# Performance work log

Hardware: AMD Instinct MI355X
Metric: run time of the kernel (lower is better)

## Reference

```python
import jax, jax.numpy as jnp
import numpy as np

B, S, D, H = 1, 4096, 1024, 16
HD = D // H

def setup_inputs() -> dict:
    key = jax.random.key(0)
    ks = jax.random.split(key, 6)
    scale = 0.02
    return {
        "x":  jax.random.normal(ks[0], (B, S, D), dtype=jnp.float32),
        "Wq": jax.random.normal(ks[1], (D, D), dtype=jnp.float32) * scale,
        "Wk": jax.random.normal(ks[2], (D, D), dtype=jnp.float32) * scale,
        "Wv": jax.random.normal(ks[3], (D, D), dtype=jnp.float32) * scale,
        "Wo": jax.random.normal(ks[4], (D, D), dtype=jnp.float32) * scale,
        "bo": jnp.zeros((D,), dtype=jnp.float32),
    }

def reference(x, Wq, Wk, Wv, Wo, bo):
    b, s, d = x.shape
    # torch Linear: y = x @ W.T (weights stored [out,in])
    def proj(W):
        return (x @ W.T).reshape(b, s, H, HD).transpose(0, 2, 1, 3)  # [b,h,s,hd]
    q, k, v = proj(Wq), proj(Wk), proj(Wv)
    scores = jnp.einsum('bhqd,bhkd->bhqk', q, k)  # [b,h,s,s]
    causal = jnp.tril(jnp.ones((s, s), dtype=bool))
    scores = jnp.where(causal, scores, -jnp.inf)
    weights = jax.nn.softmax(scores / np.sqrt(HD).astype(np.float32), axis=-1)
    ctx = jnp.einsum('bhqk,bhkd->bhqd', weights, v)
    ctx = ctx.transpose(0, 2, 1, 3).reshape(b, s, d)
    return ctx @ Wo.T + bo
```

## Files before the change

kernel.cpp:

```cpp
#include <hip/hip_runtime.h>
#include <stdint.h>

typedef unsigned short u16;
typedef __attribute__((ext_vector_type(4))) unsigned short u16x4;
typedef __attribute__((ext_vector_type(8))) unsigned short u16x8;
typedef __attribute__((ext_vector_type(8))) __bf16 bf16x8;
typedef __attribute__((ext_vector_type(4))) float f32x4;

#define S_LEN 4096
#define D_DIM 1024
#define NH    16
#define HD    64

__device__ __forceinline__ u16 f2bf(float f) {
  return __builtin_bit_cast(u16, (__bf16)f);
}
__device__ __forceinline__ float bf2f(u16 v) {
  return __builtin_bit_cast(float, (uint32_t)v << 16);
}
__device__ __forceinline__ bf16x8 bc(u16x8 v) { return __builtin_bit_cast(bf16x8, v); }
__device__ __forceinline__ float fexp2(float x) { return __builtin_amdgcn_exp2f(x); }

__device__ __forceinline__ void gload16(const u16* g, u16* l) {
  __builtin_amdgcn_global_load_lds((__attribute__((address_space(1))) void*)g,
                                   (__attribute__((address_space(3))) void*)l, 16, 0, 0);
}

__global__ __launch_bounds__(256) void conv_kernel(const float* __restrict__ src,
                                                   u16* __restrict__ dst, int n4) {
  int i = blockIdx.x * 256 + threadIdx.x;
  if (i >= n4) return;
  f32x4 v = ((const f32x4*)src)[i];
  u16x4 o;
  o[0] = f2bf(v[0]); o[1] = f2bf(v[1]); o[2] = f2bf(v[2]); o[3] = f2bf(v[3]);
  ((u16x4*)dst)[i] = o;
}

__device__ __forceinline__ void gemm_core(const u16* __restrict__ A,
                                          const u16* __restrict__ W,
                                          int m0, int n0, int Kd,
                                          u16* As, u16* Bs, f32x4 acc[4][4]) {
  const int tid  = threadIdx.x;
  const int lane = tid & 63;
  const int wv   = tid >> 6;
  const int wr   = wv >> 1, wc = wv & 1;
  const int b    = lane & 15, quad = lane >> 4;
  const int lrow = lane >> 2, lkc = (lane & 3) * 8;

  const u16* ga0 = A + (size_t)(m0 + wv * 16 + lrow) * Kd + lkc;
  const u16* ga1 = A + (size_t)(m0 + 64 + wv * 16 + lrow) * Kd + lkc;
  const u16* gb0 = W + (size_t)(n0 + wv * 16 + lrow) * Kd + lkc;
  const u16* gb1 = W + (size_t)(n0 + 64 + wv * 16 + lrow) * Kd + lkc;
  u16* la0 = As + wv * 512;
  u16* la1 = As + 2048 + wv * 512;
  u16* lb0 = Bs + wv * 512;
  u16* lb1 = Bs + 2048 + wv * 512;

  for (int k0 = 0; k0 < Kd; k0 += 32) {
    gload16(ga0 + k0, la0);
    gload16(ga1 + k0, la1);
    gload16(gb0 + k0, lb0);
    gload16(gb1 + k0, lb1);
    __syncthreads();

    u16x8 af[4], bw[4];
#pragma unroll
    for (int i = 0; i < 4; ++i) {
      af[i] = *(const u16x8*)(As + (wr * 64 + i * 16 + b) * 32 + quad * 8);
      bw[i] = *(const u16x8*)(Bs + (wc * 64 + i * 16 + b) * 32 + quad * 8);
    }
#pragma unroll
    for (int i = 0; i < 4; ++i)
#pragma unroll
      for (int j = 0; j < 4; ++j)
        acc[i][j] = __builtin_amdgcn_mfma_f32_16x16x32_bf16(bc(af[i]), bc(bw[j]), acc[i][j], 0, 0, 0);
    __syncthreads();
  }
}

__global__ __launch_bounds__(256) void gemm_qkv_kernel(const u16* __restrict__ X,
                                                       const u16* __restrict__ Wq,
                                                       const u16* __restrict__ Wk,
                                                       const u16* __restrict__ Wv,
                                                       u16* __restrict__ Q,
                                                       u16* __restrict__ K,
                                                       u16* __restrict__ Vt) {
  __shared__ __align__(16) u16 As[128 * 32];
  __shared__ __align__(16) u16 Bs[128 * 32];
  const int z = blockIdx.z;
  const u16* W = (z == 0) ? Wq : (z == 1) ? Wk : Wv;
  const int n0 = blockIdx.x * 128, m0 = blockIdx.y * 128;

  const f32x4 zero4 = {0.f, 0.f, 0.f, 0.f};
  f32x4 acc[4][4];
#pragma unroll
  for (int i = 0; i < 4; ++i)
#pragma unroll
    for (int j = 0; j < 4; ++j) acc[i][j] = zero4;

  gemm_core(X, W, m0, n0, D_DIM, As, Bs, acc);

  const int lane = threadIdx.x & 63;
  const int wv = threadIdx.x >> 6, wr = wv >> 1, wc = wv & 1;
  const int b = lane & 15, quad = lane >> 4;

  if (z < 2) {
    u16* out = (z == 0) ? Q : K;
    const float sc = (z == 0) ? 0.18033688011112042f : 1.0f;
#pragma unroll
    for (int i = 0; i < 4; ++i)
#pragma unroll
      for (int j = 0; j < 4; ++j)
#pragma unroll
        for (int r = 0; r < 4; ++r) {
          int row = m0 + wr * 64 + i * 16 + quad * 4 + r;
          int col = n0 + wc * 64 + j * 16 + b;
          out[(size_t)row * D_DIM + col] = f2bf(acc[i][j][r] * sc);
        }
  } else {
#pragma unroll
    for (int i = 0; i < 4; ++i)
#pragma unroll
      for (int j = 0; j < 4; ++j) {
        int col = n0 + wc * 64 + j * 16 + b;
        int row = m0 + wr * 64 + i * 16 + quad * 4;
        u16x4 vv;
#pragma unroll
        for (int r = 0; r < 4; ++r) vv[r] = f2bf(acc[i][j][r]);
        *(u16x4*)(Vt + (size_t)col * S_LEN + row) = vv;
      }
  }
}

__global__ __launch_bounds__(256) void attn_kernel(const u16* __restrict__ Q,
                                                   const u16* __restrict__ K,
                                                   const u16* __restrict__ Vt,
                                                   u16* __restrict__ Opart,
                                                   float* __restrict__ ml) {
  const int u = (int)gridDim.x - 1 - (int)blockIdx.x;
  const int h = u / 160;
  const int uu = u - h * 160;
  int qt, c;
  if (uu < 16)      { qt = uu;                c = 0; }
  else if (uu < 48) { qt = 16 + ((uu - 16) >> 1); c = (uu - 16) & 1; }
  else if (uu < 96) { qt = 32 + (uu - 48) / 3;    c = (uu - 48) % 3; }
  else              { qt = 48 + ((uu - 96) >> 2); c = (uu - 96) & 3; }
  const int t0 = c * 16;
  const int t_end = min(t0 + 16, qt + 1);
  const int q0 = qt * 64;

  const int tid = threadIdx.x, lane = tid & 63, w = tid >> 6;
  const int quad = lane >> 4, b = lane & 15;
  const int lrow = lane >> 2, lkc = (lane & 3) * 8;

  __shared__ __align__(16) u16 Ks[2 * 4096];
  __shared__ __align__(16) u16 Vts[2 * 4096];
  __shared__ __align__(16) u16 Ps[4][16 * 72];

  u16x8 bq[2];
  {
    const size_t qbase = (size_t)(q0 + w * 16 + b) * D_DIM + h * HD + quad * 8;
    bq[0] = *(const u16x8*)(Q + qbase);
    bq[1] = *(const u16x8*)(Q + qbase + 32);
  }

  const f32x4 zero4 = {0.f, 0.f, 0.f, 0.f};
  f32x4 o[4];
#pragma unroll
  for (int jt = 0; jt < 4; ++jt) o[jt] = zero4;
  float m_run = -3.0e38f, l_run = 0.f;

  auto stage = [&](int t, int bsel) {
    const int kv0s = t * 64;
    const u16* kg = K + (size_t)(kv0s + w * 16 + lrow) * D_DIM + h * HD + lkc;
    const u16* vg = Vt + (size_t)(h * HD + w * 16 + lrow) * S_LEN + kv0s + lkc;
    u16* kbase = Ks + bsel * 4096 + w * 512;
    u16* vbase = Vts + bsel * 4096 + w * 512;
    gload16(kg, kbase);
    gload16(kg + 32, kbase + 2048);
    gload16(vg, vbase);
    gload16(vg + 32, vbase + 2048);
  };

  u16* PsW = &Ps[w][0];
  stage(t0, 0);
  int buf = 0;

  for (int t = t0; t < t_end; ++t) {
    __syncthreads();
    if (t + 1 < t_end) stage(t + 1, buf ^ 1);
    const u16* KB = Ks + buf * 4096;
    const u16* VB = Vts + buf * 4096;

    f32x4 s[4];
#pragma unroll
    for (int jt = 0; jt < 4; ++jt) {
      s[jt] = zero4;
#pragma unroll
      for (int ks = 0; ks < 2; ++ks) {
        u16x8 ak = *(const u16x8*)(KB + ks * 2048 + (jt * 16 + b) * 32 + quad * 8);
        s[jt] = __builtin_amdgcn_mfma_f32_16x16x32_bf16(bc(ak), bc(bq[ks]), s[jt], 0, 0, 0);
      }
    }

    if (t == qt) {
      const int qg = q0 + w * 16 + b;
      const int kvb = t * 64 + quad * 4;
#pragma unroll
      for (int jt = 0; jt < 4; ++jt)
#pragma unroll
        for (int r = 0; r < 4; ++r)
          if (kvb + jt * 16 + r > qg) s[jt][r] = -1.0e30f;
    }

    float mx = s[0][0];
#pragma unroll
    for (int jt = 0; jt < 4; ++jt)
#pragma unroll
      for (int r = 0; r < 4; ++r) mx = fmaxf(mx, s[jt][r]);
    mx = fmaxf(mx, __shfl_xor(mx, 16));
    mx = fmaxf(mx, __shfl_xor(mx, 32));

    const float mn = fmaxf(m_run, mx);
    const float alpha = fexp2(m_run - mn);
    m_run = mn;

    float sum = 0.f;
#pragma unroll
    for (int jt = 0; jt < 4; ++jt) {
      u16x4 pk;
#pragma unroll
      for (int r = 0; r < 4; ++r) {
        float p = fexp2(s[jt][r] - mn);
        sum += p;
        pk[r] = f2bf(p);
      }
      *(u16x4*)(PsW + b * 72 + jt * 16 + quad * 4) = pk;
    }
    sum += __shfl_xor(sum, 16);
    sum += __shfl_xor(sum, 32);
    l_run = l_run * alpha + sum;

#pragma unroll
    for (int jt = 0; jt < 4; ++jt) o[jt] *= alpha;

    u16x8 bp[2];
    bp[0] = *(const u16x8*)(PsW + b * 72 + quad * 8);
    bp[1] = *(const u16x8*)(PsW + b * 72 + 32 + quad * 8);
#pragma unroll
    for (int jt = 0; jt < 4; ++jt)
#pragma unroll
      for (int ks = 0; ks < 2; ++ks) {
        u16x8 av = *(const u16x8*)(VB + ks * 2048 + (jt * 16 + b) * 32 + quad * 8);
        o[jt] = __builtin_amdgcn_mfma_f32_16x16x32_bf16(bc(av), bc(bp[ks]), o[jt], 0, 0, 0);
      }
    buf ^= 1;
  }

  const size_t ob = (size_t)u * 4096 + (size_t)(w * 16 + b) * 64 + quad * 4;
#pragma unroll
  for (int jt = 0; jt < 4; ++jt) {
    u16x4 ov;
#pragma unroll
    for (int r = 0; r < 4; ++r) ov[r] = f2bf(o[jt][r]);
    *(u16x4*)(Opart + ob + jt * 16) = ov;
  }
  if (quad == 0) {
    ml[(size_t)u * 128 + w * 16 + b]      = m_run;
    ml[(size_t)u * 128 + 64 + w * 16 + b] = l_run;
  }
}

__global__ __launch_bounds__(256) void attn_combine_kernel(const u16* __restrict__ Opart,
                                                           const float* __restrict__ ml,
                                                           u16* __restrict__ Ctx) {
  const int hq = blockIdx.x;
  const int h = hq >> 6, qt = hq & 63;
  int base;
  if (qt < 16)      base = qt;
  else if (qt < 32) base = 2 * qt - 16;
  else if (qt < 48) base = 3 * qt - 48;
  else              base = 4 * qt - 96;
  base += h * 160;
  const int nc = 1 + (qt >> 4);

  const int tid = threadIdx.x;
  const int row = tid >> 2;
  const int dg  = (tid & 3) * 16;

  float M = -3.0e38f;
  for (int ci = 0; ci < nc; ++ci)
    M = fmaxf(M, ml[(size_t)(base + ci) * 128 + row]);

  float L = 0.f;
  float acc[16];
#pragma unroll
  for (int i = 0; i < 16; ++i) acc[i] = 0.f;

  for (int ci = 0; ci < nc; ++ci) {
    float mp = ml[(size_t)(base + ci) * 128 + row];
    float lp = ml[(size_t)(base + ci) * 128 + 64 + row];
    float wgt = fexp2(mp - M);
    L += lp * wgt;
    const u16* op = Opart + (size_t)(base + ci) * 4096 + row * 64 + dg;
    u16x8 v0 = *(const u16x8*)op;
    u16x8 v1 = *(const u16x8*)(op + 8);
#pragma unroll
    for (int i = 0; i < 8; ++i) acc[i] += bf2f(v0[i]) * wgt;
#pragma unroll
    for (int i = 0; i < 8; ++i) acc[i + 8] += bf2f(v1[i]) * wgt;
  }
  const float inv = 1.f / L;
  u16x8 o0, o1;
#pragma unroll
  for (int i = 0; i < 8; ++i) { o0[i] = f2bf(acc[i] * inv); o1[i] = f2bf(acc[i + 8] * inv); }
  u16* dst = Ctx + (size_t)(qt * 64 + row) * D_DIM + h * HD + dg;
  *(u16x8*)dst = o0;
  *(u16x8*)(dst + 8) = o1;
}

__global__ __launch_bounds__(256) void gemm_out_kernel(const u16* __restrict__ Ctx,
                                                       const u16* __restrict__ Wo,
                                                       const float* __restrict__ bo,
                                                       float* __restrict__ out) {
  __shared__ __align__(16) u16 As[128 * 32];
  __shared__ __align__(16) u16 Bs[128 * 32];
  const int n0 = blockIdx.x * 128, m0 = blockIdx.y * 128;

  const f32x4 zero4 = {0.f, 0.f, 0.f, 0.f};
  f32x4 acc[4][4];
#pragma unroll
  for (int i = 0; i < 4; ++i)
#pragma unroll
    for (int j = 0; j < 4; ++j) acc[i][j] = zero4;

  gemm_core(Ctx, Wo, m0, n0, D_DIM, As, Bs, acc);

  const int lane = threadIdx.x & 63;
  const int wv = threadIdx.x >> 6, wr = wv >> 1, wc = wv & 1;
  const int b = lane & 15, quad = lane >> 4;

#pragma unroll
  for (int j = 0; j < 4; ++j) {
    int col = n0 + wc * 64 + j * 16 + b;
    float bias = bo[col];
#pragma unroll
    for (int i = 0; i < 4; ++i)
#pragma unroll
      for (int r = 0; r < 4; ++r) {
        int row = m0 + wr * 64 + i * 16 + quad * 4 + r;
        out[(size_t)row * D_DIM + col] = acc[i][j][r] + bias;
      }
  }
}

extern "C" void kernel_launch(void* const* d_in, const int* in_sizes, int n_in,
                              void* d_out, int out_size, void* d_ws, size_t ws_size,
                              hipStream_t stream) {
  const float* x  = (const float*)d_in[0];
  const float* Wq = (const float*)d_in[1];
  const float* Wk = (const float*)d_in[2];
  const float* Wv = (const float*)d_in[3];
  const float* Wo = (const float*)d_in[4];
  const float* bo = (const float*)d_in[5];
  float* out = (float*)d_out;

  char* ws = (char*)d_ws;
  const size_t MB = 1u << 20;
  u16*   Xb    = (u16*)(ws + 0 * MB);
  u16*   Wqb   = (u16*)(ws + 8 * MB);
  u16*   Wkb   = (u16*)(ws + 10 * MB);
  u16*   Wvb   = (u16*)(ws + 12 * MB);
  u16*   Wob   = (u16*)(ws + 14 * MB);
  u16*   Qb    = (u16*)(ws + 16 * MB);
  u16*   Kb    = (u16*)(ws + 24 * MB);
  u16*   Vtb   = (u16*)(ws + 32 * MB);
  u16*   Cxb   = (u16*)(ws + 40 * MB);
  u16*   Opart = (u16*)(ws + 48 * MB);
  float* mlbuf = (float*)(ws + 68 * MB);

  conv_kernel<<<4096, 256, 0, stream>>>(x,  Xb,  (S_LEN * D_DIM) / 4);
  conv_kernel<<<1024, 256, 0, stream>>>(Wq, Wqb, (D_DIM * D_DIM) / 4);
  conv_kernel<<<1024, 256, 0, stream>>>(Wk, Wkb, (D_DIM * D_DIM) / 4);
  conv_kernel<<<1024, 256, 0, stream>>>(Wv, Wvb, (D_DIM * D_DIM) / 4);
  conv_kernel<<<1024, 256, 0, stream>>>(Wo, Wob, (D_DIM * D_DIM) / 4);

  gemm_qkv_kernel<<<dim3(D_DIM / 128, S_LEN / 128, 3), 256, 0, stream>>>(
      Xb, Wqb, Wkb, Wvb, Qb, Kb, Vtb);

  attn_kernel<<<dim3(2560), 256, 0, stream>>>(Qb, Kb, Vtb, Opart, mlbuf);

  attn_combine_kernel<<<dim3(1024), 256, 0, stream>>>(Opart, mlbuf, Cxb);

  gemm_out_kernel<<<dim3(D_DIM / 128, S_LEN / 128), 256, 0, stream>>>(Cxb, Wob, bo, out);
}
```

Baseline: 248.8 us.

## Use 128-row query tiles in attention, swizzle LDS, fuse conversion launches

Result: faster. 214.1 us (-13.9%).

```diff
diff --git a/kernel.cpp b/kernel.cpp
--- a/kernel.cpp
+++ b/kernel.cpp
@@ -26,10 +26,26 @@
                                    (__attribute__((address_space(3))) void*)l, 16, 0, 0);
 }
 
-__global__ __launch_bounds__(256) void conv_kernel(const float* __restrict__ src,
-                                                   u16* __restrict__ dst, int n4) {
-  int i = blockIdx.x * 256 + threadIdx.x;
-  if (i >= n4) return;
+__global__ __launch_bounds__(256) void conv_all_kernel(const float* __restrict__ x,
+                                                       const float* __restrict__ Wq,
+                                                       const float* __restrict__ Wk,
+                                                       const float* __restrict__ Wv,
+                                                       const float* __restrict__ Wo,
+                                                       u16* __restrict__ Xb, u16* __restrict__ Wqb,
+                                                       u16* __restrict__ Wkb, u16* __restrict__ Wvb,
+                                                       u16* __restrict__ Wob) {
+  int blk = blockIdx.x;
+  const float* src;
+  u16* dst;
+  int i;
+  if (blk < 4096) { src = x; dst = Xb; i = blk * 256 + threadIdx.x; }
+  else {
+    int wi = (blk - 4096) >> 10;
+    int lb = (blk - 4096) & 1023;
+    src = (wi == 0) ? Wq : (wi == 1) ? Wk : (wi == 2) ? Wv : Wo;
+    dst = (wi == 0) ? Wqb : (wi == 1) ? Wkb : (wi == 2) ? Wvb : Wob;
+    i = lb * 256 + threadIdx.x;
+  }
   f32x4 v = ((const f32x4*)src)[i];
   u16x4 o;
   o[0] = f2bf(v[0]); o[1] = f2bf(v[1]); o[2] = f2bf(v[2]); o[3] = f2bf(v[3]);
@@ -45,12 +61,14 @@
   const int wv   = tid >> 6;
   const int wr   = wv >> 1, wc = wv & 1;
   const int b    = lane & 15, quad = lane >> 4;
-  const int lrow = lane >> 2, lkc = (lane & 3) * 8;
-
-  const u16* ga0 = A + (size_t)(m0 + wv * 16 + lrow) * Kd + lkc;
-  const u16* ga1 = A + (size_t)(m0 + 64 + wv * 16 + lrow) * Kd + lkc;
-  const u16* gb0 = W + (size_t)(n0 + wv * 16 + lrow) * Kd + lkc;
-  const u16* gb1 = W + (size_t)(n0 + 64 + wv * 16 + lrow) * Kd + lkc;
+  const int lrow = lane >> 2;
+  const int cg   = ((lane & 3) - (lrow >> 1)) & 3;
+  const int goff = ((quad + (b >> 1)) & 3) * 8;
+
+  const u16* ga0 = A + (size_t)(m0 + wv * 16 + lrow) * Kd + cg * 8;
+  const u16* ga1 = A + (size_t)(m0 + 64 + wv * 16 + lrow) * Kd + cg * 8;
+  const u16* gb0 = W + (size_t)(n0 + wv * 16 + lrow) * Kd + cg * 8;
+  const u16* gb1 = W + (size_t)(n0 + 64 + wv * 16 + lrow) * Kd + cg * 8;
   u16* la0 = As + wv * 512;
   u16* la1 = As + 2048 + wv * 512;
   u16* lb0 = Bs + wv * 512;
@@ -66,8 +84,8 @@
     u16x8 af[4], bw[4];
 #pragma unroll
     for (int i = 0; i < 4; ++i) {
-      af[i] = *(const u16x8*)(As + (wr * 64 + i * 16 + b) * 32 + quad * 8);
-      bw[i] = *(const u16x8*)(Bs + (wc * 64 + i * 16 + b) * 32 + quad * 8);
+      af[i] = *(const u16x8*)(As + (wr * 64 + i * 16 + b) * 32 + goff);
+      bw[i] = *(const u16x8*)(Bs + (wc * 64 + i * 16 + b) * 32 + goff);
     }
 #pragma unroll
     for (int i = 0; i < 4; ++i)
@@ -132,30 +150,38 @@
   }
 }
 
-__global__ __launch_bounds__(256) void attn_kernel(const u16* __restrict__ Q,
+__global__ __launch_bounds__(512) void attn_kernel(const u16* __restrict__ Q,
                                                    const u16* __restrict__ K,
                                                    const u16* __restrict__ Vt,
                                                    u16* __restrict__ Opart,
                                                    float* __restrict__ ml) {
   const int u = (int)gridDim.x - 1 - (int)blockIdx.x;
-  const int h = u / 160;
-  const int uu = u - h * 160;
+  const int h = u / 80;
+  const int uu = u - h * 80;
   int qt, c;
-  if (uu < 16)      { qt = uu;                c = 0; }
-  else if (uu < 48) { qt = 16 + ((uu - 16) >> 1); c = (uu - 16) & 1; }
-  else if (uu < 96) { qt = 32 + (uu - 48) / 3;    c = (uu - 48) % 3; }
-  else              { qt = 48 + ((uu - 96) >> 2); c = (uu - 96) & 3; }
+  if (uu < 8)       { qt = uu;                    c = 0; }
+  else if (uu < 24) { qt = 8 + ((uu - 8) >> 1);   c = (uu - 8) & 1; }
+  else if (uu < 48) { qt = 16 + (uu - 24) / 3;    c = (uu - 24) % 3; }
+  else              { qt = 24 + ((uu - 48) >> 2); c = (uu - 48) & 3; }
   const int t0 = c * 16;
-  const int t_end = min(t0 + 16, qt + 1);
-  const int q0 = qt * 64;
+  const int t_end = min(t0 + 16, 2 * qt + 2);
+  const int q0 = qt * 128;
 
   const int tid = threadIdx.x, lane = tid & 63, w = tid >> 6;
   const int quad = lane >> 4, b = lane & 15;
-  const int lrow = lane >> 2, lkc = (lane & 3) * 8;
+  const int lrow = lane >> 2;
+  const int cg   = ((lane & 3) - (lrow >> 1)) & 3;
+  const int goff = ((quad + (b >> 1)) & 3) * 8;
 
   __shared__ __align__(16) u16 Ks[2 * 4096];
   __shared__ __align__(16) u16 Vts[2 * 4096];
-  __shared__ __align__(16) u16 Ps[4][16 * 72];
+  __shared__ __align__(16) u16 Ps[8][16 * 72];
+
+  const int ksg = w & 1, rg = w >> 1;
+  const u16* kgb = K + (size_t)(rg * 16 + lrow) * D_DIM + h * HD + ksg * 32 + cg * 8;
+  const u16* vgb = Vt + (size_t)(h * HD + rg * 16 + lrow) * S_LEN + ksg * 32 + cg * 8;
+  u16* const ldk = Ks + ksg * 2048 + rg * 512;
+  u16* const ldv = Vts + ksg * 2048 + rg * 512;
 
   u16x8 bq[2];
   {
@@ -171,93 +197,90 @@
   float m_run = -3.0e38f, l_run = 0.f;
 
   auto stage = [&](int t, int bsel) {
-    const int kv0s = t * 64;
-    const u16* kg = K + (size_t)(kv0s + w * 16 + lrow) * D_DIM + h * HD + lkc;
-    const u16* vg = Vt + (size_t)(h * HD + w * 16 + lrow) * S_LEN + kv0s + lkc;
-    u16* kbase = Ks + bsel * 4096 + w * 512;
-    u16* vbase = Vts + bsel * 4096 + w * 512;
-    gload16(kg, kbase);
-    gload16(kg + 32, kbase + 2048);
-    gload16(vg, vbase);
-    gload16(vg + 32, vbase + 2048);
+    gload16(kgb + (size_t)t * 64 * D_DIM, ldk + bsel * 4096);
+    gload16(vgb + t * 64, ldv + bsel * 4096);
   };
 
   u16* PsW = &Ps[w][0];
+  const int qg = q0 + w * 16 + b;
+  const int qg_wmax = q0 + w * 16 + 15;
   stage(t0, 0);
   int buf = 0;
 
   for (int t = t0; t < t_end; ++t) {
     __syncthreads();
     if (t + 1 < t_end) stage(t + 1, buf ^ 1);
-    const u16* KB = Ks + buf * 4096;
-    const u16* VB = Vts + buf * 4096;
-
-    f32x4 s[4];
-#pragma unroll
-    for (int jt = 0; jt < 4; ++jt) {
-      s[jt] = zero4;
-#pragma unroll
-      for (int ks = 0; ks < 2; ++ks) {
-        u16x8 ak = *(const u16x8*)(KB + ks * 2048 + (jt * 16 + b) * 32 + quad * 8);
-        s[jt] = __builtin_amdgcn_mfma_f32_16x16x32_bf16(bc(ak), bc(bq[ks]), s[jt], 0, 0, 0);
+
+    if (t * 64 <= qg_wmax) {
+      const u16* KB = Ks + buf * 4096;
+      const u16* VB = Vts + buf * 4096;
+
+      f32x4 s[4];
+#pragma unroll
+      for (int jt = 0; jt < 4; ++jt) {
+        s[jt] = zero4;
+#pragma unroll
+        for (int ks = 0; ks < 2; ++ks) {
+          u16x8 ak = *(const u16x8*)(KB + ks * 2048 + jt * 512 + b * 32 + goff);
+          s[jt] = __builtin_amdgcn_mfma_f32_16x16x32_bf16(bc(ak), bc(bq[ks]), s[jt], 0, 0, 0);
+        }
       }
+
+      if (t * 64 + 63 > qg) {
+        const int kvb = t * 64 + quad * 4;
+#pragma unroll
+        for (int jt = 0; jt < 4; ++jt)
+#pragma unroll
+          for (int r = 0; r < 4; ++r)
+            if (kvb + jt * 16 + r > qg) s[jt][r] = -1.0e30f;
+      }
+
+      float mx = s[0][0];
+#pragma unroll
+      for (int jt = 0; jt < 4; ++jt)
+#pragma unroll
+        for (int r = 0; r < 4; ++r) mx = fmaxf(mx, s[jt][r]);
+      mx = fmaxf(mx, __shfl_xor(mx, 16));
+      mx = fmaxf(mx, __shfl_xor(mx, 32));
+
+      const float mn = fmaxf(m_run, mx);
+      const float alpha = fexp2(m_run - mn);
+      m_run = mn;
+
+      float sum = 0.f;
+#pragma unroll
+      for (int jt = 0; jt < 4; ++jt) {
+        u16x4 pk;
+#pragma unroll
+        for (int r = 0; r < 4; ++r) {
+          float p = fexp2(s[jt][r] - mn);
+          sum += p;
+          pk[r] = f2bf(p);
+        }
+        *(u16x4*)(PsW + b * 72 + jt * 16 + quad * 4) = pk;
+      }
+      sum += __shfl_xor(sum, 16);
+      sum += __shfl_xor(sum, 32);
+      l_run = l_run * alpha + sum;
+
+#pragma unroll
+      for (int jt = 0; jt < 4; ++jt) o[jt] *= alpha;
+
+      u16x8 bp[2];
+      bp[0] = *(const u16x8*)(PsW + b * 72 + quad * 8);
+      bp[1] = *(const u16x8*)(PsW + b * 72 + 32 + quad * 8);
+#pragma unroll
+      for (int jt = 0; jt < 4; ++jt)
+#pragma unroll
+        for (int ks = 0; ks < 2; ++ks) {
+          u16x8 av = *(const u16x8*)(VB + ks * 2048 + jt * 512 + b * 32 + goff);
+          o[jt] = __builtin_amdgcn_mfma_f32_16x16x32_bf16(bc(av), bc(bp[ks]), o[jt], 0, 0, 0);
+        }
     }
-
-    if (t == qt) {
-      const int qg = q0 + w * 16 + b;
-      const int kvb = t * 64 + quad * 4;
-#pragma unroll
-      for (int jt = 0; jt < 4; ++jt)
-#pragma unroll
-        for (int r = 0; r < 4; ++r)
-          if (kvb + jt * 16 + r > qg) s[jt][r] = -1.0e30f;
-    }
-
-    float mx = s[0][0];
-#pragma unroll
-    for (int jt = 0; jt < 4; ++jt)
-#pragma unroll
-      for (int r = 0; r < 4; ++r) mx = fmaxf(mx, s[jt][r]);
-    mx = fmaxf(mx, __shfl_xor(mx, 16));
-    mx = fmaxf(mx, __shfl_xor(mx, 32));
-
-    const float mn = fmaxf(m_run, mx);
-    const float alpha = fexp2(m_run - mn);
-    m_run = mn;
-
-    float sum = 0.f;
-#pragma unroll
-    for (int jt = 0; jt < 4; ++jt) {
-      u16x4 pk;
-#pragma unroll
-      for (int r = 0; r < 4; ++r) {
-        float p = fexp2(s[jt][r] - mn);
-        sum += p;
-        pk[r] = f2bf(p);
-      }
-      *(u16x4*)(PsW + b * 72 + jt * 16 + quad * 4) = pk;
-    }
-    sum += __shfl_xor(sum, 16);
-    sum += __shfl_xor(sum, 32);
-    l_run = l_run * alpha + sum;
-
-#pragma unroll
-    for (int jt = 0; jt < 4; ++jt) o[jt] *= alpha;
-
-    u16x8 bp[2];
-    bp[0] = *(const u16x8*)(PsW + b * 72 + quad * 8);
-    bp[1] = *(const u16x8*)(PsW + b * 72 + 32 + quad * 8);
-#pragma unroll
-    for (int jt = 0; jt < 4; ++jt)
-#pragma unroll
-      for (int ks = 0; ks < 2; ++ks) {
-        u16x8 av = *(const u16x8*)(VB + ks * 2048 + (jt * 16 + b) * 32 + quad * 8);
-        o[jt] = __builtin_amdgcn_mfma_f32_16x16x32_bf16(bc(av), bc(bp[ks]), o[jt], 0, 0, 0);
-      }
     buf ^= 1;
   }
 
-  const size_t ob = (size_t)u * 4096 + (size_t)(w * 16 + b) * 64 + quad * 4;
+  const size_t ob = (size_t)u * 8192 + (size_t)(w * 16 + b) * 64 + quad * 4;
 #pragma unroll
   for (int jt = 0; jt < 4; ++jt) {
     u16x4 ov;
@@ -266,8 +289,8 @@
     *(u16x4*)(Opart + ob + jt * 16) = ov;
   }
   if (quad == 0) {
-    ml[(size_t)u * 128 + w * 16 + b]      = m_run;
-    ml[(size_t)u * 128 + 64 + w * 16 + b] = l_run;
+    ml[(size_t)u * 256 + w * 16 + b]       = m_run;
+    ml[(size_t)u * 256 + 128 + w * 16 + b] = l_run;
   }
 }
 
@@ -275,22 +298,24 @@
                                                            const float* __restrict__ ml,
                                                            u16* __restrict__ Ctx) {
   const int hq = blockIdx.x;
-  const int h = hq >> 6, qt = hq & 63;
+  const int h = hq >> 6, qt64 = hq & 63;
+  const int qt = qt64 >> 1;
   int base;
-  if (qt < 16)      base = qt;
-  else if (qt < 32) base = 2 * qt - 16;
-  else if (qt < 48) base = 3 * qt - 48;
-  else              base = 4 * qt - 96;
-  base += h * 160;
-  const int nc = 1 + (qt >> 4);
+  if (qt < 8)       base = qt;
+  else if (qt < 16) base = 2 * qt - 8;
+  else if (qt < 24) base = 3 * qt - 24;
+  else              base = 4 * qt - 48;
+  base += h * 80;
+  const int nc = 1 + (qt >> 3);
 
   const int tid = threadIdx.x;
   const int row = tid >> 2;
+  const int urow = (qt64 & 1) * 64 + row;
   const int dg  = (tid & 3) * 16;
 
   float M = -3.0e38f;
   for (int ci = 0; ci < nc; ++ci)
-    M = fmaxf(M, ml[(size_t)(base + ci) * 128 + row]);
+    M = fmaxf(M, ml[(size_t)(base + ci) * 256 + urow]);
 
   float L = 0.f;
   float acc[16];
@@ -298,11 +323,11 @@
   for (int i = 0; i < 16; ++i) acc[i] = 0.f;
 
   for (int ci = 0; ci < nc; ++ci) {
-    float mp = ml[(size_t)(base + ci) * 128 + row];
-    float lp = ml[(size_t)(base + ci) * 128 + 64 + row];
+    float mp = ml[(size_t)(base + ci) * 256 + urow];
+    float lp = ml[(size_t)(base + ci) * 256 + 128 + urow];
     float wgt = fexp2(mp - M);
     L += lp * wgt;
-    const u16* op = Opart + (size_t)(base + ci) * 4096 + row * 64 + dg;
+    const u16* op = Opart + (size_t)(base + ci) * 8192 + (size_t)urow * 64 + dg;
     u16x8 v0 = *(const u16x8*)op;
     u16x8 v1 = *(const u16x8*)(op + 8);
 #pragma unroll
@@ -314,7 +339,7 @@
   u16x8 o0, o1;
 #pragma unroll
   for (int i = 0; i < 8; ++i) { o0[i] = f2bf(acc[i] * inv); o1[i] = f2bf(acc[i + 8] * inv); }
-  u16* dst = Ctx + (size_t)(qt * 64 + row) * D_DIM + h * HD + dg;
+  u16* dst = Ctx + (size_t)(qt64 * 64 + row) * D_DIM + h * HD + dg;
   *(u16x8*)dst = o0;
   *(u16x8*)(dst + 8) = o1;
 }
@@ -379,16 +404,12 @@
   u16*   Opart = (u16*)(ws + 48 * MB);
   float* mlbuf = (float*)(ws + 68 * MB);
 
-  conv_kernel<<<4096, 256, 0, stream>>>(x,  Xb,  (S_LEN * D_DIM) / 4);
-  conv_kernel<<<1024, 256, 0, stream>>>(Wq, Wqb, (D_DIM * D_DIM) / 4);
-  conv_kernel<<<1024, 256, 0, stream>>>(Wk, Wkb, (D_DIM * D_DIM) / 4);
-  conv_kernel<<<1024, 256, 0, stream>>>(Wv, Wvb, (D_DIM * D_DIM) / 4);
-  conv_kernel<<<1024, 256, 0, stream>>>(Wo, Wob, (D_DIM * D_DIM) / 4);
+  conv_all_kernel<<<8192, 256, 0, stream>>>(x, Wq, Wk, Wv, Wo, Xb, Wqb, Wkb, Wvb, Wob);
 
   gemm_qkv_kernel<<<dim3(D_DIM / 128, S_LEN / 128, 3), 256, 0, stream>>>(
       Xb, Wqb, Wkb, Wvb, Qb, Kb, Vtb);
 
-  attn_kernel<<<dim3(2560), 256, 0, stream>>>(Qb, Kb, Vtb, Opart, mlbuf);
+  attn_kernel<<<dim3(1280), 512, 0, stream>>>(Qb, Kb, Vtb, Opart, mlbuf);
 
   attn_combine_kernel<<<dim3(1024), 256, 0, stream>>>(Opart, mlbuf, Cxb);
 
```
